# Optimization experiments

Measured on AMD Instinct MI355X. Metric: run time of the kernel, lower is better.

Reference implementation:

```python
import jax, jax.numpy as jnp
import numpy as np

NUM_FEAS = 4096
HID = 128
BATCH = 128


def setup_inputs() -> dict:
    key = jax.random.key(0)
    k1, k2, k3, k4 = jax.random.split(key, 4)
    batch_x = jax.random.normal(k1, (BATCH, NUM_FEAS), dtype=jnp.float32)
    C = jax.random.normal(k2, (1, HID), dtype=jnp.float32)
    W = jax.random.normal(k3, (NUM_FEAS, HID), dtype=jnp.float32)
    B = jax.random.normal(k4, (NUM_FEAS,), dtype=jnp.float32)
    return {"batch_x": batch_x, "C": C, "W": W, "B": B}


def reference(batch_x, C, W, B):
    # binarize input (matches (x > 0).float())
    x = (batch_x > 0).astype(jnp.float32)  # [B, F]
    # prefix sums: S_excl[b, i] = sum_{j < i} x[b, j] * W[j]   -> [B, F, H]
    contrib = x[:, :, None] * W[None, :, :]
    S = jnp.cumsum(contrib, axis=1)
    S_excl = jnp.concatenate([jnp.zeros_like(S[:, :1]), S[:, :-1]], axis=1)
    # hidden state for i >= 1: h_i = sigmoid(S_excl_i + C)
    h = jax.nn.sigmoid(S_excl + C[None, :, :])  # [B, F, H]
    # faithful quirk: for i == 0 the original uses raw C (no sigmoid)
    h = h.at[:, 0, :].set(jnp.broadcast_to(C[0], (x.shape[0], HID)))
    # logits z_i = h_i . W_i + B_i ; p_i = sigmoid(z_i)
    z = jnp.einsum('bfh,fh->bf', h, W) + B[None, :]
    # BCE(sum over features), stable via log_sigmoid
    log_p = jax.nn.log_sigmoid(z)
    log_q = jax.nn.log_sigmoid(-z)
    loss_per_sample = -jnp.sum(x * log_p + (1.0 - x) * log_q, axis=1)
    return jnp.mean(loss_per_sample)
```

## Files before the change

### kernel.cpp

```cpp
#include <hip/hip_runtime.h>

#define NFEAS 4096
#define HID   128
#define BATCH 128
#define NSUB  64
#define NC    16
#define KF    256
#define L2E   1.4426950408889634f
#define LN2   0.6931471805599453f

__device__ __forceinline__ float scan64(float v) {
  float r = v; int y;
  y = __builtin_amdgcn_update_dpp(0, __float_as_int(r), 0x111, 0xF, 0xF, true); r += __int_as_float(y);
  y = __builtin_amdgcn_update_dpp(0, __float_as_int(r), 0x112, 0xF, 0xF, true); r += __int_as_float(y);
  y = __builtin_amdgcn_update_dpp(0, __float_as_int(r), 0x114, 0xF, 0xF, true); r += __int_as_float(y);
  y = __builtin_amdgcn_update_dpp(0, __float_as_int(r), 0x118, 0xF, 0xF, true); r += __int_as_float(y);
  y = __builtin_amdgcn_update_dpp(0, __float_as_int(r), 0x142, 0xA, 0xF, true); r += __int_as_float(y);
  y = __builtin_amdgcn_update_dpp(0, __float_as_int(r), 0x143, 0xC, 0xF, true); r += __int_as_float(y);
  return r;
}

__device__ __forceinline__ void scan64_x4(float& a, float& b, float& c, float& d) {
  int t0, t1, t2, t3;
#define S4(ctrl, rm)                                                              \
  t0 = __builtin_amdgcn_update_dpp(0, __float_as_int(a), ctrl, rm, 0xF, true);    \
  t1 = __builtin_amdgcn_update_dpp(0, __float_as_int(b), ctrl, rm, 0xF, true);    \
  t2 = __builtin_amdgcn_update_dpp(0, __float_as_int(c), ctrl, rm, 0xF, true);    \
  t3 = __builtin_amdgcn_update_dpp(0, __float_as_int(d), ctrl, rm, 0xF, true);    \
  a += __int_as_float(t0); b += __int_as_float(t1);                               \
  c += __int_as_float(t2); d += __int_as_float(t3);
  S4(0x111, 0xF) S4(0x112, 0xF) S4(0x114, 0xF) S4(0x118, 0xF)
  S4(0x142, 0xA) S4(0x143, 0xC)
#undef S4
}

__global__ __launch_bounds__(128) void chunk_sums_kernel(
    const float* __restrict__ x, const float* __restrict__ W,
    float* __restrict__ T)
{
  __shared__ float xm[64][8];
  const int c = blockIdx.x, g = blockIdx.y, t = threadIdx.x;

  {
    const int s = t >> 4, fb = (t & 15) << 2;
    const float4 v = *reinterpret_cast<const float4*>(
        &x[(size_t)(g * 8 + s) * NFEAS + c * 64 + fb]);
    xm[fb + 0][s] = v.x > 0.f ? 1.f : 0.f;
    xm[fb + 1][s] = v.y > 0.f ? 1.f : 0.f;
    xm[fb + 2][s] = v.z > 0.f ? 1.f : 0.f;
    xm[fb + 3][s] = v.w > 0.f ? 1.f : 0.f;
  }
  __syncthreads();

  float acc[8];
  #pragma unroll
  for (int s = 0; s < 8; ++s) acc[s] = 0.f;

  #pragma unroll 4
  for (int f = 0; f < 64; ++f) {
    const float wv = W[(size_t)(c * 64 + f) * HID + t];
    const float4 ma = *reinterpret_cast<const float4*>(&xm[f][0]);
    const float4 mb = *reinterpret_cast<const float4*>(&xm[f][4]);
    acc[0] = __builtin_fmaf(ma.x, wv, acc[0]);
    acc[1] = __builtin_fmaf(ma.y, wv, acc[1]);
    acc[2] = __builtin_fmaf(ma.z, wv, acc[2]);
    acc[3] = __builtin_fmaf(ma.w, wv, acc[3]);
    acc[4] = __builtin_fmaf(mb.x, wv, acc[4]);
    acc[5] = __builtin_fmaf(mb.y, wv, acc[5]);
    acc[6] = __builtin_fmaf(mb.z, wv, acc[6]);
    acc[7] = __builtin_fmaf(mb.w, wv, acc[7]);
  }
  #pragma unroll
  for (int s = 0; s < 8; ++s)
    T[((size_t)(g * 8 + s) * HID + t) * NSUB + c] = acc[s];
}

__global__ __launch_bounds__(256) void prefix_kernel(float* __restrict__ T)
{
  const int gw = blockIdx.x * 4 + (threadIdx.x >> 6);
  const int lane = threadIdx.x & 63;
  float* p = T + (size_t)gw * NSUB;
  const float v = p[lane];
  const float r = scan64(v);
  p[lane] = r - v;
}

__global__ __launch_bounds__(512, 4) void scan_loss_kernel(
    const float* __restrict__ x,  const float* __restrict__ Cv,
    const float* __restrict__ W,  const float* __restrict__ Bv,
    const float* __restrict__ T,  float* __restrict__ losses)
{
  __shared__ float wt[32 * 256];
  __shared__ float s2m[HID];
  __shared__ float s2r[HID];
  __shared__ float lred[8];

  const int tid = threadIdx.x;
  const int b = blockIdx.x, c = blockIdx.y;
  const int base = c * KF;
  const int lane = tid & 63, w = tid >> 6;

  if (tid < HID) {
    const float s2 = T[((size_t)b * HID + tid) * NSUB + c * 4] + Cv[tid];
    s2r[tid] = s2;
    s2m[tid] = -L2E * s2;
  }

  const float4 xv = *reinterpret_cast<const float4*>(
      x + (size_t)b * NFEAS + base + 4 * lane);
  const float xm0 = xv.x > 0.f ? 1.f : 0.f;
  const float xm1 = xv.y > 0.f ? 1.f : 0.f;
  const float xm2 = xv.z > 0.f ? 1.f : 0.f;
  const float xm3 = xv.w > 0.f ? 1.f : 0.f;

  float z0 = 0.f, z1 = 0.f, z2 = 0.f, z3 = 0.f;

  const int hb = tid & 7;
  const int f0 = tid >> 3;
  const int colw = f0 ^ ((hb & 3) << 3);
  const float* wbase = W + (size_t)base * HID;
  const bool quirk = (c == 0);

  for (int hq = 0; hq < 4; ++hq) {
    if (hq) __syncthreads();
    #pragma unroll
    for (int k = 0; k < 4; ++k) {
      const int f = f0 + (k << 6);
      const float4 v = *reinterpret_cast<const float4*>(
          wbase + (size_t)f * HID + (hq << 5) + (hb << 2));
      float* wp = &wt[((hb << 2) << 8) + colw + (k << 6)];
      wp[0]   = v.x;
      wp[256] = v.y;
      wp[512] = v.z;
      wp[768] = v.w;
    }
    __syncthreads();

    const int hl0 = w << 2;
    const int colx = (lane << 2) ^ ((w & 3) << 3);
    const float4 wv0 = *reinterpret_cast<const float4*>(&wt[(hl0 + 0) * 256 + colx]);
    const float4 wv1 = *reinterpret_cast<const float4*>(&wt[(hl0 + 1) * 256 + colx]);
    const float4 wv2 = *reinterpret_cast<const float4*>(&wt[(hl0 + 2) * 256 + colx]);
    const float4 wv3 = *reinterpret_cast<const float4*>(&wt[(hl0 + 3) * 256 + colx]);
    const float4 sm4 = *reinterpret_cast<const float4*>(&s2m[(hq << 5) + hl0]);

    const float m00 = wv0.x * xm0, m01 = wv0.y * xm1, m02 = wv0.z * xm2, m03 = wv0.w * xm3;
    const float m10 = wv1.x * xm0, m11 = wv1.y * xm1, m12 = wv1.z * xm2, m13 = wv1.w * xm3;
    const float m20 = wv2.x * xm0, m21 = wv2.y * xm1, m22 = wv2.z * xm2, m23 = wv2.w * xm3;
    const float m30 = wv3.x * xm0, m31 = wv3.y * xm1, m32 = wv3.z * xm2, m33 = wv3.w * xm3;

    const float ps0 = (m00 + m01) + (m02 + m03);
    const float ps1 = (m10 + m11) + (m12 + m13);
    const float ps2 = (m20 + m21) + (m22 + m23);
    const float ps3 = (m30 + m31) + (m32 + m33);

    float r0 = ps0, r1 = ps1, r2 = ps2, r3 = ps3;
    scan64_x4(r0, r1, r2, r3);

#define CHAIN(J, wvJ, rJ, psJ, mJ0, mJ1, mJ2, smJ)                                          \
    {                                                                                        \
      const float e0 = rJ - psJ;                                                             \
      const float e1 = e0 + mJ0;                                                             \
      const float e2 = e1 + mJ1;                                                             \
      const float e3 = e2 + mJ2;                                                             \
      float g0 = __builtin_amdgcn_rcpf(1.f + __builtin_amdgcn_exp2f(__builtin_fmaf(e0, -L2E, smJ))); \
      const float g1 = __builtin_amdgcn_rcpf(1.f + __builtin_amdgcn_exp2f(__builtin_fmaf(e1, -L2E, smJ))); \
      const float g2 = __builtin_amdgcn_rcpf(1.f + __builtin_amdgcn_exp2f(__builtin_fmaf(e2, -L2E, smJ))); \
      const float g3 = __builtin_amdgcn_rcpf(1.f + __builtin_amdgcn_exp2f(__builtin_fmaf(e3, -L2E, smJ))); \
      if (quirk && lane == 0) g0 = s2r[(hq << 5) + hl0 + J];                                 \
      z0 = __builtin_fmaf(g0, wvJ.x, z0);                                                    \
      z1 = __builtin_fmaf(g1, wvJ.y, z1);                                                    \
      z2 = __builtin_fmaf(g2, wvJ.z, z2);                                                    \
      z3 = __builtin_fmaf(g3, wvJ.w, z3);                                                    \
    }
    CHAIN(0, wv0, r0, ps0, m00, m01, m02, sm4.x)
    CHAIN(1, wv1, r1, ps1, m10, m11, m12, sm4.y)
    CHAIN(2, wv2, r2, ps2, m20, m21, m22, sm4.z)
    CHAIN(3, wv3, r3, ps3, m30, m31, m32, sm4.w)
#undef CHAIN
  }

  __syncthreads();
  {
    float4 zv; zv.x = z0; zv.y = z1; zv.z = z2; zv.w = z3;
    *reinterpret_cast<float4*>(&wt[w * 256 + 4 * lane]) = zv;
  }
  __syncthreads();

  if (tid < 256) {
    float zt = 0.f;
    #pragma unroll
    for (int ww = 0; ww < 8; ++ww) zt += wt[ww * 256 + tid];
    zt += Bv[base + tid];
    const float xf = x[(size_t)b * NFEAS + base + tid] > 0.f ? 1.f : 0.f;
    const float az = __builtin_fabsf(zt);
    const float ee = __builtin_amdgcn_exp2f(-L2E * az);
    const float li = fmaxf(zt, 0.f) - xf * zt +
                     LN2 * __builtin_amdgcn_logf(1.f + ee);
    const float tot = scan64(li);
    if ((tid & 63) == 63) lred[tid >> 6] = tot;
  }
  __syncthreads();
  if (tid == 0)
    losses[b * NC + c] = (lred[0] + lred[1]) + (lred[2] + lred[3]);
}

__global__ __launch_bounds__(256) void finalize_kernel(
    const float* __restrict__ losses, float* __restrict__ out)
{
  __shared__ float sm[256];
  const int t = threadIdx.x;
  float s = 0.f;
  for (int i = t; i < BATCH * NC; i += 256) s += losses[i];
  sm[t] = s;
  __syncthreads();
  for (int w = 128; w > 0; w >>= 1) {
    if (t < w) sm[t] += sm[t + w];
    __syncthreads();
  }
  if (t == 0) out[0] = sm[0] * (1.f / BATCH);
}

extern "C" void kernel_launch(void* const* d_in, const int* in_sizes, int n_in,
                              void* d_out, int out_size, void* d_ws, size_t ws_size,
                              hipStream_t stream)
{
  const float* x  = (const float*)d_in[0];
  const float* Cv = (const float*)d_in[1];
  const float* W  = (const float*)d_in[2];
  const float* Bv = (const float*)d_in[3];
  float* out = (float*)d_out;

  float* T      = (float*)d_ws;
  float* losses = T + (size_t)BATCH * HID * NSUB;

  chunk_sums_kernel<<<dim3(NSUB, BATCH / 8), 128, 0, stream>>>(x, W, T);
  prefix_kernel<<<dim3(BATCH * HID / 4), 256, 0, stream>>>(T);
  scan_loss_kernel<<<dim3(BATCH, NC), 512, 0, stream>>>(x, Cv, W, Bv, T, losses);
  finalize_kernel<<<1, 256, 0, stream>>>(losses, out);
}
```

Baseline: 55.24 us.

## Restructure scan-loss into W-tile-reused zpart kernel plus separate BCE reduction

The per-(batch, chunk) scan_loss kernel, which reloaded a W tile into shared memory four times per block, is replaced by a zpart kernel indexed by (chunk, hidden quarter, batch group). Each block loads one 32-column W tile once and reuses it across 8 batch rows, one per wave. Partial logits per hidden quarter go to global memory, and a new bce_kernel sums the four partials, adds the bias, computes the per-sample BCE and reduces it. The prefix kernel now writes the scaled per-chunk start state directly. This cuts W traffic and barriers but adds a 4×B×F partial-logit round trip through global memory and an extra launch.

```diff
diff --git a/kernel.cpp b/kernel.cpp
--- a/kernel.cpp
+++ b/kernel.cpp
@@ -4,7 +4,7 @@
 #define HID   128
 #define BATCH 128
 #define NSUB  64
-#define NC    16
+#define NCH   16
 #define KF    256
 #define L2E   1.4426950408889634f
 #define LN2   0.6931471805599453f
@@ -75,74 +75,73 @@
     T[((size_t)(g * 8 + s) * HID + t) * NSUB + c] = acc[s];
 }
 
-__global__ __launch_bounds__(256) void prefix_kernel(float* __restrict__ T)
+__global__ __launch_bounds__(256) void prefix_s2m_kernel(
+    const float* __restrict__ T, const float* __restrict__ Cv,
+    float* __restrict__ s2m)
 {
   const int gw = blockIdx.x * 4 + (threadIdx.x >> 6);
   const int lane = threadIdx.x & 63;
-  float* p = T + (size_t)gw * NSUB;
-  const float v = p[lane];
+  const int h = gw & 127;
+  const float v = T[(size_t)gw * NSUB + lane];
   const float r = scan64(v);
-  p[lane] = r - v;
-}
-
-__global__ __launch_bounds__(512, 4) void scan_loss_kernel(
-    const float* __restrict__ x,  const float* __restrict__ Cv,
-    const float* __restrict__ W,  const float* __restrict__ Bv,
-    const float* __restrict__ T,  float* __restrict__ losses)
+  if ((lane & 3) == 0) {
+    const float excl = r - v;
+    s2m[(size_t)(lane >> 2) * (BATCH * HID) + gw] = -L2E * (excl + Cv[h]);
+  }
+}
+
+__global__ __launch_bounds__(512, 6) void zpart_kernel(
+    const float* __restrict__ x,   const float* __restrict__ W,
+    const float* __restrict__ Cv,  const float* __restrict__ s2m,
+    float* __restrict__ zpart)
 {
   __shared__ float wt[32 * 256];
-  __shared__ float s2m[HID];
-  __shared__ float s2r[HID];
-  __shared__ float lred[8];
-
-  const int tid = threadIdx.x;
-  const int b = blockIdx.x, c = blockIdx.y;
+  __shared__ float s2l[8 * 32];
+  __shared__ float cvl[32];
+
+  const int c  = blockIdx.x;
+  const int hq = blockIdx.y;
+  const int bg = blockIdx.z;
+  const int tid = threadIdx.x, lane = tid & 63, w = tid >> 6;
   const int base = c * KF;
-  const int lane = tid & 63, w = tid >> 6;
-
-  if (tid < HID) {
-    const float s2 = T[((size_t)b * HID + tid) * NSUB + c * 4] + Cv[tid];
-    s2r[tid] = s2;
-    s2m[tid] = -L2E * s2;
-  }
-
+
+  {
+    const int hb = tid & 7, f0 = tid >> 3;
+    const float* wp = W + (size_t)(base + f0) * HID + (hq << 5) + (hb << 2);
+    const int colw = f0 ^ ((hb & 3) << 3);
+    #pragma unroll
+    for (int k = 0; k < 4; ++k) {
+      const float4 v = *reinterpret_cast<const float4*>(wp + (size_t)(k << 6) * HID);
+      float* q = &wt[((hb << 2) << 8) + colw + (k << 6)];
+      q[0] = v.x; q[256] = v.y; q[512] = v.z; q[768] = v.w;
+    }
+  }
+  if (tid < 256) {
+    s2l[tid] = s2m[(size_t)c * (BATCH * HID) +
+                   (size_t)(bg * 8 + (tid >> 5)) * HID + (hq << 5) + (tid & 31)];
+  }
+  if (tid < 32) cvl[tid] = Cv[(hq << 5) + tid];
+  __syncthreads();
+
+  const int b = bg * 8 + w;
   const float4 xv = *reinterpret_cast<const float4*>(
-      x + (size_t)b * NFEAS + base + 4 * lane);
+      x + (size_t)b * NFEAS + base + (lane << 2));
   const float xm0 = xv.x > 0.f ? 1.f : 0.f;
   const float xm1 = xv.y > 0.f ? 1.f : 0.f;
   const float xm2 = xv.z > 0.f ? 1.f : 0.f;
   const float xm3 = xv.w > 0.f ? 1.f : 0.f;
+  const bool qk = (c == 0) && (lane == 0);
 
   float z0 = 0.f, z1 = 0.f, z2 = 0.f, z3 = 0.f;
 
-  const int hb = tid & 7;
-  const int f0 = tid >> 3;
-  const int colw = f0 ^ ((hb & 3) << 3);
-  const float* wbase = W + (size_t)base * HID;
-  const bool quirk = (c == 0);
-
-  for (int hq = 0; hq < 4; ++hq) {
-    if (hq) __syncthreads();
-    #pragma unroll
-    for (int k = 0; k < 4; ++k) {
-      const int f = f0 + (k << 6);
-      const float4 v = *reinterpret_cast<const float4*>(
-          wbase + (size_t)f * HID + (hq << 5) + (hb << 2));
-      float* wp = &wt[((hb << 2) << 8) + colw + (k << 6)];
-      wp[0]   = v.x;
-      wp[256] = v.y;
-      wp[512] = v.z;
-      wp[768] = v.w;
-    }
-    __syncthreads();
-
-    const int hl0 = w << 2;
-    const int colx = (lane << 2) ^ ((w & 3) << 3);
-    const float4 wv0 = *reinterpret_cast<const float4*>(&wt[(hl0 + 0) * 256 + colx]);
-    const float4 wv1 = *reinterpret_cast<const float4*>(&wt[(hl0 + 1) * 256 + colx]);
-    const float4 wv2 = *reinterpret_cast<const float4*>(&wt[(hl0 + 2) * 256 + colx]);
-    const float4 wv3 = *reinterpret_cast<const float4*>(&wt[(hl0 + 3) * 256 + colx]);
-    const float4 sm4 = *reinterpret_cast<const float4*>(&s2m[(hq << 5) + hl0]);
+  #pragma unroll
+  for (int cg = 0; cg < 8; ++cg) {
+    const int colx = (lane << 2) ^ ((cg & 3) << 3);
+    const int rb = (cg << 2) * 256 + colx;
+    const float4 wv0 = *reinterpret_cast<const float4*>(&wt[rb]);
+    const float4 wv1 = *reinterpret_cast<const float4*>(&wt[rb + 256]);
+    const float4 wv2 = *reinterpret_cast<const float4*>(&wt[rb + 512]);
+    const float4 wv3 = *reinterpret_cast<const float4*>(&wt[rb + 768]);
 
     const float m00 = wv0.x * xm0, m01 = wv0.y * xm1, m02 = wv0.z * xm2, m03 = wv0.w * xm3;
     const float m10 = wv1.x * xm0, m11 = wv1.y * xm1, m12 = wv1.z * xm2, m13 = wv1.w * xm3;
@@ -157,8 +156,10 @@
     float r0 = ps0, r1 = ps1, r2 = ps2, r3 = ps3;
     scan64_x4(r0, r1, r2, r3);
 
-#define CHAIN(J, wvJ, rJ, psJ, mJ0, mJ1, mJ2, smJ)                                          \
+#define CHAIN(J, wvJ, rJ, psJ, mJ0, mJ1, mJ2)                                               \
     {                                                                                        \
+      const int ch = (cg << 2) + J;                                                          \
+      const float smJ = s2l[(w << 5) + ch];                                                  \
       const float e0 = rJ - psJ;                                                             \
       const float e1 = e0 + mJ0;                                                             \
       const float e2 = e1 + mJ1;                                                             \
@@ -167,55 +168,61 @@
       const float g1 = __builtin_amdgcn_rcpf(1.f + __builtin_amdgcn_exp2f(__builtin_fmaf(e1, -L2E, smJ))); \
       const float g2 = __builtin_amdgcn_rcpf(1.f + __builtin_amdgcn_exp2f(__builtin_fmaf(e2, -L2E, smJ))); \
       const float g3 = __builtin_amdgcn_rcpf(1.f + __builtin_amdgcn_exp2f(__builtin_fmaf(e3, -L2E, smJ))); \
-      if (quirk && lane == 0) g0 = s2r[(hq << 5) + hl0 + J];                                 \
+      if (qk) g0 = cvl[ch];                                   \
       z0 = __builtin_fmaf(g0, wvJ.x, z0);                                                    \
       z1 = __builtin_fmaf(g1, wvJ.y, z1);                                                    \
       z2 = __builtin_fmaf(g2, wvJ.z, z2);                                                    \
       z3 = __builtin_fmaf(g3, wvJ.w, z3);                                                    \
     }
-    CHAIN(0, wv0, r0, ps0, m00, m01, m02, sm4.x)
-    CHAIN(1, wv1, r1, ps1, m10, m11, m12, sm4.y)
-    CHAIN(2, wv2, r2, ps2, m20, m21, m22, sm4.z)
-    CHAIN(3, wv3, r3, ps3, m30, m31, m32, sm4.w)
+    CHAIN(0, wv0, r0, ps0, m00, m01, m02)
+    CHAIN(1, wv1, r1, ps1, m10, m11, m12)
+    CHAIN(2, wv2, r2, ps2, m20, m21, m22)
+    CHAIN(3, wv3, r3, ps3, m30, m31, m32)
 #undef CHAIN
   }
 
-  __syncthreads();
-  {
-    float4 zv; zv.x = z0; zv.y = z1; zv.z = z2; zv.w = z3;
-    *reinterpret_cast<float4*>(&wt[w * 256 + 4 * lane]) = zv;
-  }
-  __syncthreads();
-
-  if (tid < 256) {
-    float zt = 0.f;
-    #pragma unroll
-    for (int ww = 0; ww < 8; ++ww) zt += wt[ww * 256 + tid];
-    zt += Bv[base + tid];
-    const float xf = x[(size_t)b * NFEAS + base + tid] > 0.f ? 1.f : 0.f;
+  float4 zv; zv.x = z0; zv.y = z1; zv.z = z2; zv.w = z3;
+  *reinterpret_cast<float4*>(
+      &zpart[((size_t)hq * BATCH + b) * NFEAS + base + (lane << 2)]) = zv;
+}
+
+__global__ __launch_bounds__(256) void bce_kernel(
+    const float* __restrict__ x, const float* __restrict__ Bv,
+    const float* __restrict__ zpart, float* __restrict__ lossb)
+{
+  __shared__ float sm[256];
+  const int b = blockIdx.x, t = threadIdx.x;
+  const size_t Q = (size_t)BATCH * NFEAS;
+  float acc = 0.f;
+  #pragma unroll
+  for (int i = 0; i < NFEAS / 256; ++i) {
+    const int f = i * 256 + t;
+    const size_t o = (size_t)b * NFEAS + f;
+    const float zt = ((zpart[o] + zpart[Q + o]) +
+                      (zpart[2 * Q + o] + zpart[3 * Q + o])) + Bv[f];
+    const float xf = x[o] > 0.f ? 1.f : 0.f;
     const float az = __builtin_fabsf(zt);
     const float ee = __builtin_amdgcn_exp2f(-L2E * az);
-    const float li = fmaxf(zt, 0.f) - xf * zt +
-                     LN2 * __builtin_amdgcn_logf(1.f + ee);
-    const float tot = scan64(li);
-    if ((tid & 63) == 63) lred[tid >> 6] = tot;
-  }
-  __syncthreads();
-  if (tid == 0)
-    losses[b * NC + c] = (lred[0] + lred[1]) + (lred[2] + lred[3]);
-}
-
-__global__ __launch_bounds__(256) void finalize_kernel(
-    const float* __restrict__ losses, float* __restrict__ out)
-{
-  __shared__ float sm[256];
+    acc += fmaxf(zt, 0.f) - xf * zt + LN2 * __builtin_amdgcn_logf(1.f + ee);
+  }
+  sm[t] = acc;
+  __syncthreads();
+  for (int s = 128; s > 0; s >>= 1) {
+    if (t < s) sm[t] += sm[t + s];
+    __syncthreads();
+  }
+  if (t == 0) lossb[b] = sm[0];
+}
+
+__global__ __launch_bounds__(128) void finalize_kernel(
+    const float* __restrict__ lossb, float* __restrict__ out)
+{
+  __shared__ float sm[128];
   const int t = threadIdx.x;
-  float s = 0.f;
-  for (int i = t; i < BATCH * NC; i += 256) s += losses[i];
-  sm[t] = s;
-  __syncthreads();
-  for (int w = 128; w > 0; w >>= 1) {
-    if (t < w) sm[t] += sm[t + w];
+  sm[t] = lossb[t];
+  __syncthreads();
+  for (int s = 64; s > 0; s >>= 1) {
+    if (t < s) sm[t] += sm[t + s];
     __syncthreads();
   }
   if (t == 0) out[0] = sm[0] * (1.f / BATCH);
@@ -231,11 +238,14 @@
   const float* Bv = (const float*)d_in[3];
   float* out = (float*)d_out;
 
-  float* T      = (float*)d_ws;
-  float* losses = T + (size_t)BATCH * HID * NSUB;
+  float* T     = (float*)d_ws;
+  float* s2m   = T     + (size_t)BATCH * HID * NSUB;
+  float* zpart = s2m   + (size_t)NCH * BATCH * HID;
+  float* lossb = zpart + (size_t)4 * BATCH * NFEAS;
 
   chunk_sums_kernel<<<dim3(NSUB, BATCH / 8), 128, 0, stream>>>(x, W, T);
-  prefix_kernel<<<dim3(BATCH * HID / 4), 256, 0, stream>>>(T);
-  scan_loss_kernel<<<dim3(BATCH, NC), 512, 0, stream>>>(x, Cv, W, Bv, T, losses);
-  finalize_kernel<<<1, 256, 0, stream>>>(losses, out);
-}
+  prefix_s2m_kernel<<<dim3(BATCH * HID / 4), 256, 0, stream>>>(T, Cv, s2m);
+  zpart_kernel<<<dim3(NCH, 4, BATCH / 8), 512, 0, stream>>>(x, W, Cv, s2m, zpart);
+  bce_kernel<<<dim3(BATCH), 256, 0, stream>>>(x, Bv, zpart, lossb);
+  finalize_kernel<<<1, 128, 0, stream>>>(lossb, out);
+}
```

Result: slower. 57.68 us (+4.4%).
